# Performance work log

Hardware: AMD Instinct MI355X
Metric: run time of the kernel (lower is better)

Reference implementation:

```python
import jax, jax.numpy as jnp
import numpy as np


def setup_inputs() -> dict:
    key = jax.random.key(0)
    ks = jax.random.split(key, 9)
    B, S, E, H, D = 8, 1000, 1024, 16, 64
    sc = 0.02
    return {
        "x": jax.random.normal(ks[0], (B, S, E), dtype=jnp.float32),
        "wq": jax.random.normal(ks[1], (H, E, D), dtype=jnp.float32) * sc,
        "bq": jax.random.normal(ks[2], (H, D), dtype=jnp.float32) * sc,
        "wk": jax.random.normal(ks[3], (H, E, D), dtype=jnp.float32) * sc,
        "bk": jax.random.normal(ks[4], (H, D), dtype=jnp.float32) * sc,
        "wv": jax.random.normal(ks[5], (H, E, D), dtype=jnp.float32) * sc,
        "bv": jax.random.normal(ks[6], (H, D), dtype=jnp.float32) * sc,
        "wp": jax.random.normal(ks[7], (E, E), dtype=jnp.float32) * sc,
        "bp": jax.random.normal(ks[8], (E,), dtype=jnp.float32) * sc,
    }


def reference(x, wq, bq, wk, bk, wv, bv, wp, bp):
    B, S, E = x.shape
    H, _, D = wq.shape
    # per-head projections, all heads batched: [B,H,S,D]
    q = jnp.einsum('bse,hed->bhsd', x, wq) + bq[None, :, None, :]
    k = jnp.einsum('bse,hed->bhsd', x, wk) + bk[None, :, None, :]
    v = jnp.einsum('bse,hed->bhsd', x, wv) + bv[None, :, None, :]
    # NOTE: original scales by sqrt(seq_len), not sqrt(head_dim)
    scores = jnp.einsum('bhsd,bhtd->bhst', q, k) / jnp.asarray(S, x.dtype) ** 0.5
    causal = jnp.tril(jnp.ones((S, S), dtype=bool))  # mask[:S,:S] == 1 keeps
    scores = jnp.where(causal, scores, jnp.asarray(-jnp.inf, x.dtype))
    attn = jax.nn.softmax(scores, axis=-1)
    z = jnp.einsum('bhst,bhtd->bhsd', attn, v)
    # concat heads in head order -> [B,S,E]
    y = z.transpose(0, 2, 1, 3).reshape(B, S, E)
    # projection then exact GELU (dropout is identity at eval)
    return jax.nn.gelu(jnp.einsum('bse,ef->bsf', y, wp) + bp, approximate=False)
```

## Files before the change

kernel.cpp:

```cpp
#include <hip/hip_runtime.h>
#include <hip/hip_bf16.h>
#include <math.h>

constexpr int B_ = 8, S_ = 1000, E_ = 1024, H_ = 16, D_ = 64;
constexpr int M_ = B_ * S_;

using bf16x8 = __attribute__((ext_vector_type(8))) __bf16;
using u16x8  = __attribute__((ext_vector_type(8))) unsigned short;
using f32x4  = __attribute__((ext_vector_type(4))) float;

static __device__ __forceinline__ unsigned short f2bf(float f) {
    union { float f; unsigned u; } c; c.f = f;
    return (unsigned short)((c.u + 0x7FFF + ((c.u >> 16) & 1)) >> 16);
}
static __device__ __forceinline__ unsigned short f2bf_fast(float f) {
    union { float f; unsigned u; } c; c.f = f;
    return (unsigned short)((c.u + 0x8000) >> 16);
}
static __device__ __forceinline__ float bfr2f(unsigned short s) {
    union { unsigned u; float f; } c; c.u = ((unsigned)s) << 16;
    return c.f;
}

static __device__ __forceinline__ void gld16(const unsigned short* g, unsigned short* lds) {
    __builtin_amdgcn_global_load_lds(
        (__attribute__((address_space(1))) void*)(g),
        (__attribute__((address_space(3))) void*)(lds), 16, 0, 0);
}

__global__ __launch_bounds__(256) void cast_x_kernel(
    const float* __restrict__ x, unsigned short* __restrict__ xbf)
{
    const size_t i = ((size_t)blockIdx.x * 256 + threadIdx.x) * 4;
    float4 v = *(const float4*)(x + i);
    ushort4 o;
    o.x = f2bf(v.x); o.y = f2bf(v.y); o.z = f2bf(v.z); o.w = f2bf(v.w);
    *(ushort4*)(xbf + i) = o;
}

__global__ __launch_bounds__(256) void transpose_wqkv_kernel(
    const float* __restrict__ wq, const float* __restrict__ wk,
    const float* __restrict__ wv, unsigned short* __restrict__ WT)
{
    __shared__ unsigned short Ts[64 * 65];
    const int et = blockIdx.x, zh = blockIdx.y;
    const int z = zh >> 4, h = zh & 15;
    const float* src = (z == 0 ? wq : z == 1 ? wk : wv) + (size_t)h * E_ * D_;

    const int d = threadIdx.x & 63;
    const int e0 = threadIdx.x >> 6;
    #pragma unroll
    for (int p = 0; p < 16; ++p) {
        const int e = e0 + p * 4;
        Ts[d * 65 + e] = f2bf(src[(size_t)(et * 64 + e) * D_ + d]);
    }
    __syncthreads();
    const int e = threadIdx.x & 63;
    const int d0 = threadIdx.x >> 6;
    #pragma unroll
    for (int p = 0; p < 16; ++p) {
        const int dd = d0 + p * 4;
        WT[((size_t)zh * 64 + dd) * E_ + et * 64 + e] = Ts[dd * 65 + e];
    }
}

__global__ __launch_bounds__(256) void transpose_wp_kernel(
    const float* __restrict__ wp, unsigned short* __restrict__ wpT)
{
    __shared__ unsigned short Ts[64 * 65];
    const int et = blockIdx.x, ft = blockIdx.y;
    const int f = threadIdx.x & 63;
    const int e0 = threadIdx.x >> 6;
    #pragma unroll
    for (int p = 0; p < 16; ++p) {
        const int e = e0 + p * 4;
        Ts[f * 65 + e] = f2bf(wp[(size_t)(et * 64 + e) * E_ + ft * 64 + f]);
    }
    __syncthreads();
    const int e = threadIdx.x & 63;
    const int f0 = threadIdx.x >> 6;
    #pragma unroll
    for (int p = 0; p < 16; ++p) {
        const int ff = f0 + p * 4;
        wpT[((size_t)(ft * 64 + ff)) * E_ + et * 64 + e] = Ts[ff * 65 + e];
    }
}

__global__ __launch_bounds__(256) void transpose_v_kernel(
    const unsigned short* __restrict__ vb, unsigned short* __restrict__ vt)
{
    __shared__ unsigned short Ts[64 * 65];
    const int st = blockIdx.x, bh = blockIdx.y;
    const size_t ibase = (size_t)bh * S_ * D_;
    const size_t obase = (size_t)bh * D_ * S_;

    const int d = threadIdx.x & 63;
    const int s0 = threadIdx.x >> 6;
    #pragma unroll
    for (int p = 0; p < 16; ++p) {
        const int s = s0 + p * 4;
        const int srow = st * 64 + s;
        Ts[s * 65 + d] = (srow < S_) ? vb[ibase + (size_t)srow * D_ + d] : 0;
    }
    __syncthreads();
    const int s = threadIdx.x & 63;
    const int d0 = threadIdx.x >> 6;
    const int scol = st * 64 + s;
    if (scol < S_) {
        #pragma unroll
        for (int p = 0; p < 16; ++p) {
            const int dd = d0 + p * 4;
            vt[obase + (size_t)dd * S_ + scol] = Ts[s * 65 + dd];
        }
    }
}

__global__ __launch_bounds__(256) void qkv_mfma_kernel(
    const unsigned short* __restrict__ xbf, const unsigned short* __restrict__ WT,
    const float* __restrict__ bq, const float* __restrict__ bk,
    const float* __restrict__ bv,
    unsigned short* __restrict__ qb, unsigned short* __restrict__ kb,
    unsigned short* __restrict__ vb)
{
    __shared__ unsigned short As[128 * 64];
    __shared__ unsigned short Bs[128 * 64];

    const int tid  = threadIdx.x;
    const int wave = tid >> 6, lane = tid & 63;
    const int m16  = lane & 15, quad = lane >> 4;
    const int wm   = wave >> 1, wn = wave & 1;
    const int n0   = blockIdx.x * 128;
    const int m0   = blockIdx.y * 128;

    f32x4 acc[4][4];
    #pragma unroll
    for (int nf = 0; nf < 4; ++nf)
        #pragma unroll
        for (int mf = 0; mf < 4; ++mf)
            acc[nf][mf] = (f32x4){0.f, 0.f, 0.f, 0.f};

    const int lrow = lane >> 3;
    const int lcol = (lane & 7) << 3;

    int a_srow[4];
    #pragma unroll
    for (int j = 0; j < 4; ++j) {
        int r = m0 + (wave * 4 + j) * 8 + lrow;
        a_srow[j] = (r < M_) ? r : (M_ - 1);
    }

    for (int kk = 0; kk < E_; kk += 64) {
        __syncthreads();
        #pragma unroll
        for (int j = 0; j < 4; ++j) {
            const int i = wave * 4 + j;
            gld16(xbf + (size_t)a_srow[j] * E_ + kk + lcol, &As[i * 512]);
            gld16(WT + (size_t)(n0 + i * 8 + lrow) * E_ + kk + lcol, &Bs[i * 512]);
        }
        __syncthreads();

        #pragma unroll
        for (int kh = 0; kh < 2; ++kh) {
            const int ko = kh * 32 + quad * 8;
            bf16x8 af[4];
            #pragma unroll
            for (int mf = 0; mf < 4; ++mf)
                af[mf] = *(const bf16x8*)&As[(wm * 64 + mf * 16 + m16) * 64 + ko];
            #pragma unroll
            for (int nf = 0; nf < 4; ++nf) {
                const bf16x8 bfr = *(const bf16x8*)&Bs[(wn * 64 + nf * 16 + m16) * 64 + ko];
                #pragma unroll
                for (int mf = 0; mf < 4; ++mf)
                    acc[nf][mf] = __builtin_amdgcn_mfma_f32_16x16x32_bf16(
                        af[mf], bfr, acc[nf][mf], 0, 0, 0);
            }
        }
    }

    const int z = n0 >> 10;
    const int h = ((n0 >> 6) + wn) & 15;
    unsigned short* const ob = (z == 0) ? qb : (z == 1) ? kb : vb;
    const float* const bz    = (z == 0) ? bq : (z == 1) ? bk : bv;

    float biasv[4];
    #pragma unroll
    for (int nf = 0; nf < 4; ++nf)
        biasv[nf] = bz[h * D_ + nf * 16 + m16];

    #pragma unroll
    for (int mf = 0; mf < 4; ++mf)
        #pragma unroll
        for (int r = 0; r < 4; ++r) {
            const int row = m0 + wm * 64 + mf * 16 + quad * 4 + r;
            if (row < M_) {
                const int b = row / S_, s = row % S_;
                const size_t obase = (((size_t)b * H_ + h) * S_ + s) * D_ + m16;
                #pragma unroll
                for (int nf = 0; nf < 4; ++nf)
                    ob[obase + nf * 16] = f2bf(acc[nf][mf][r] + biasv[nf]);
            }
        }
}

__global__ __launch_bounds__(256) void attn_flash_kernel(
    const unsigned short* __restrict__ q, const unsigned short* __restrict__ k,
    const unsigned short* __restrict__ vt, unsigned short* __restrict__ ybf)
{
    constexpr int P_ = 72;
    __shared__ unsigned short Qs[64 * P_];
    __shared__ unsigned short Ks[64 * P_];
    __shared__ unsigned short Vt[64 * P_];
    __shared__ unsigned short Ps[4][16 * P_];

    const int tid  = threadIdx.x;
    const int wave = tid >> 6, lane = tid & 63;
    const int m16  = lane & 15, quad = lane >> 4;
    const int qt = (int)gridDim.x - 1 - (int)blockIdx.x;
    const int h = blockIdx.y, b = blockIdx.z;
    const size_t bh  = ((size_t)b * H_ + h) * S_;
    const size_t vtb = ((size_t)b * H_ + h) * (size_t)D_ * S_;
    const float sl2e = 0.031622776601683794f * 1.4426950408889634f;

    const int c8 = (tid & 7) * 8;
    const int r0 = tid >> 3;

    #pragma unroll
    for (int rr = 0; rr < 64; rr += 32) {
        const int r = r0 + rr;
        const int srow = qt * 64 + r;
        u16x8 val = {0, 0, 0, 0, 0, 0, 0, 0};
        if (srow < S_) val = *(const u16x8*)(q + (bh + srow) * D_ + c8);
        u16x8 o;
        #pragma unroll
        for (int j = 0; j < 8; ++j) o[j] = f2bf_fast(bfr2f(val[j]) * sl2e);
        *(u16x8*)&Qs[r * P_ + c8] = o;
    }
    __syncthreads();

    const bf16x8 qa0 = *(const bf16x8*)&Qs[(wave * 16 + m16) * P_ + quad * 8];
    const bf16x8 qa1 = *(const bf16x8*)&Qs[(wave * 16 + m16) * P_ + 32 + quad * 8];

    f32x4 O[4] = {{0,0,0,0},{0,0,0,0},{0,0,0,0},{0,0,0,0}};
    float l_i[4] = {0.f, 0.f, 0.f, 0.f};

    const int qrow_base = qt * 64 + wave * 16 + quad * 4;

    u16x8 kreg[2], vreg[2];
    #pragma unroll
    for (int i = 0; i < 2; ++i) {
        const int srow = r0 + i * 32;
        kreg[i] = *(const u16x8*)(k + (bh + srow) * D_ + c8);
        vreg[i] = *(const u16x8*)(vt + vtb + (size_t)(r0 + i * 32) * S_ + c8);
    }

    for (int tt = 0; tt <= qt; ++tt) {
        const int t0 = tt * 64;
        __syncthreads();
        #pragma unroll
        for (int i = 0; i < 2; ++i) {
            *(u16x8*)&Ks[(r0 + i * 32) * P_ + c8] = kreg[i];
            *(u16x8*)&Vt[(r0 + i * 32) * P_ + c8] = vreg[i];
        }
        __syncthreads();

        if (tt < qt) {
            const int nt0 = t0 + 64;
            #pragma unroll
            for (int i = 0; i < 2; ++i) {
                const int t = r0 + i * 32;
                const int srow = nt0 + t;
                u16x8 kv = {0,0,0,0,0,0,0,0}, vv = {0,0,0,0,0,0,0,0};
                if (srow < S_) kv = *(const u16x8*)(k + (bh + srow) * D_ + c8);
                if (nt0 + c8 < S_)
                    vv = *(const u16x8*)(vt + vtb + (size_t)t * S_ + nt0 + c8);
                kreg[i] = kv; vreg[i] = vv;
            }
        }

        f32x4 sc[4];
        #pragma unroll
        for (int ts = 0; ts < 4; ++ts) {
            const bf16x8 kb0 = *(const bf16x8*)&Ks[(ts * 16 + m16) * P_ + quad * 8];
            const bf16x8 kb1 = *(const bf16x8*)&Ks[(ts * 16 + m16) * P_ + 32 + quad * 8];
            f32x4 a = {0.f, 0.f, 0.f, 0.f};
            a = __builtin_amdgcn_mfma_f32_16x16x32_bf16(qa0, kb0, a, 0, 0, 0);
            a = __builtin_amdgcn_mfma_f32_16x16x32_bf16(qa1, kb1, a, 0, 0, 0);
            sc[ts] = a;
        }

        unsigned short* const pw = &Ps[wave][0];
        if (tt == qt) {
            #pragma unroll
            for (int ts = 0; ts < 4; ++ts) {
                const int t = t0 + ts * 16 + m16;
                #pragma unroll
                for (int r = 0; r < 4; ++r) {
                    float p = __builtin_amdgcn_exp2f(sc[ts][r]);
                    p = (t <= qrow_base + r) ? p : 0.f;
                    pw[(quad * 4 + r) * P_ + ts * 16 + m16] = f2bf_fast(p);
                    l_i[r] += p;
                }
            }
        } else {
            #pragma unroll
            for (int ts = 0; ts < 4; ++ts)
                #pragma unroll
                for (int r = 0; r < 4; ++r) {
                    const float p = __builtin_amdgcn_exp2f(sc[ts][r]);
                    pw[(quad * 4 + r) * P_ + ts * 16 + m16] = f2bf_fast(p);
                    l_i[r] += p;
                }
        }

        const bf16x8 pa0 = *(const bf16x8*)&pw[m16 * P_ + quad * 8];
        const bf16x8 pa1 = *(const bf16x8*)&pw[m16 * P_ + 32 + quad * 8];
        #pragma unroll
        for (int db = 0; db < 4; ++db) {
            const bf16x8 vb0 = *(const bf16x8*)&Vt[(db * 16 + m16) * P_ + quad * 8];
            const bf16x8 vb1 = *(const bf16x8*)&Vt[(db * 16 + m16) * P_ + 32 + quad * 8];
            O[db] = __builtin_amdgcn_mfma_f32_16x16x32_bf16(pa0, vb0, O[db], 0, 0, 0);
            O[db] = __builtin_amdgcn_mfma_f32_16x16x32_bf16(pa1, vb1, O[db], 0, 0, 0);
        }
    }

    #pragma unroll
    for (int off = 1; off < 16; off <<= 1)
        #pragma unroll
        for (int r = 0; r < 4; ++r)
            l_i[r] += __shfl_xor(l_i[r], off, 64);

    #pragma unroll
    for (int r = 0; r < 4; ++r) {
        const int qrow = qrow_base + r;
        if (qrow < S_) {
            const float invl = 1.0f / l_i[r];
            #pragma unroll
            for (int db = 0; db < 4; ++db)
                ybf[((size_t)b * S_ + qrow) * E_ + h * D_ + db * 16 + m16] =
                    f2bf(O[db][r] * invl);
        }
    }
}

__global__ __launch_bounds__(256) void proj_mfma_kernel(
    const unsigned short* __restrict__ ybf, const unsigned short* __restrict__ wpT,
    const float* __restrict__ bp, float* __restrict__ out)
{
    constexpr int P = 72;
    __shared__ unsigned short As[128 * P];
    __shared__ unsigned short Bs[128 * P];

    const int tid = threadIdx.x;
    const int wave = tid >> 6, lane = tid & 63;
    const int m16 = lane & 15, quad = lane >> 4;
    const int wm = wave >> 1, wn = wave & 1;
    const int m0 = blockIdx.x * 128;
    const int n0 = blockIdx.y * 128;

    f32x4 acc[4][4];
    #pragma unroll
    for (int nf = 0; nf < 4; ++nf)
        #pragma unroll
        for (int mf = 0; mf < 4; ++mf)
            acc[nf][mf] = (f32x4){0.f, 0.f, 0.f, 0.f};

    const int ar = tid & 31;
    const int ac8 = (tid >> 5) * 8;

    int asrow[4];
    #pragma unroll
    for (int p = 0; p < 4; ++p) {
        int r = m0 + ar + p * 32;
        asrow[p] = (r < M_) ? r : (M_ - 1);
    }

    u16x8 areg[4], breg[4];
    #pragma unroll
    for (int p = 0; p < 4; ++p) {
        areg[p] = *(const u16x8*)(ybf + (size_t)asrow[p] * E_ + ac8);
        breg[p] = *(const u16x8*)(wpT + (size_t)(n0 + ar + p * 32) * E_ + ac8);
    }

    for (int kk = 0; kk < E_; kk += 64) {
        __syncthreads();
        #pragma unroll
        for (int p = 0; p < 4; ++p) {
            *(u16x8*)&As[(ar + p * 32) * P + ac8] = areg[p];
            *(u16x8*)&Bs[(ar + p * 32) * P + ac8] = breg[p];
        }
        __syncthreads();

        if (kk + 64 < E_) {
            const int kn = kk + 64;
            #pragma unroll
            for (int p = 0; p < 4; ++p) {
                areg[p] = *(const u16x8*)(ybf + (size_t)asrow[p] * E_ + kn + ac8);
                breg[p] = *(const u16x8*)(wpT + (size_t)(n0 + ar + p * 32) * E_ + kn + ac8);
            }
        }

        #pragma unroll
        for (int kh = 0; kh < 2; ++kh) {
            const int ko = kh * 32 + quad * 8;
            bf16x8 af[4];
            #pragma unroll
            for (int mf = 0; mf < 4; ++mf)
                af[mf] = *(const bf16x8*)&As[(wm * 64 + mf * 16 + m16) * P + ko];
            #pragma unroll
            for (int nf = 0; nf < 4; ++nf) {
                const bf16x8 bfr = *(const bf16x8*)&Bs[(wn * 64 + nf * 16 + m16) * P + ko];
                #pragma unroll
                for (int mf = 0; mf < 4; ++mf)
                    acc[nf][mf] = __builtin_amdgcn_mfma_f32_16x16x32_bf16(
                        af[mf], bfr, acc[nf][mf], 0, 0, 0);
            }
        }
    }

    float biasv[4];
    #pragma unroll
    for (int nf = 0; nf < 4; ++nf)
        biasv[nf] = bp[n0 + wn * 64 + nf * 16 + m16];

    #pragma unroll
    for (int mf = 0; mf < 4; ++mf)
        #pragma unroll
        for (int r = 0; r < 4; ++r) {
            const int row = m0 + wm * 64 + mf * 16 + quad * 4 + r;
            if (row < M_) {
                #pragma unroll
                for (int nf = 0; nf < 4; ++nf) {
                    const int col = n0 + wn * 64 + nf * 16 + m16;
                    const float t = acc[nf][mf][r] + biasv[nf];
                    const float g = 0.5f * t * (1.0f + erff(t * 0.70710678118654752f));
                    out[(size_t)row * E_ + col] = g;
                }
            }
        }
}

extern "C" void kernel_launch(void* const* d_in, const int* in_sizes, int n_in,
                              void* d_out, int out_size, void* d_ws, size_t ws_size,
                              hipStream_t stream)
{
    const float* x  = (const float*)d_in[0];
    const float* wq = (const float*)d_in[1];
    const float* bq = (const float*)d_in[2];
    const float* wk = (const float*)d_in[3];
    const float* bk = (const float*)d_in[4];
    const float* wv = (const float*)d_in[5];
    const float* bv = (const float*)d_in[6];
    const float* wp = (const float*)d_in[7];
    const float* bp = (const float*)d_in[8];
    float* out = (float*)d_out;

    const size_t nME = (size_t)M_ * E_;
    unsigned short* xbf = (unsigned short*)d_ws;
    unsigned short* WT  = xbf + nME;
    unsigned short* wpT = WT + 3145728;
    unsigned short* qb  = wpT + 1048576;
    unsigned short* kb  = qb + nME;
    unsigned short* vb  = kb + nME;
    unsigned short* ybf = vb + nME;
    unsigned short* vtr = ybf + nME;

    cast_x_kernel<<<dim3((unsigned)(nME / 1024)), 256, 0, stream>>>(x, xbf);
    transpose_wqkv_kernel<<<dim3(16, 48), 256, 0, stream>>>(wq, wk, wv, WT);
    transpose_wp_kernel<<<dim3(16, 16), 256, 0, stream>>>(wp, wpT);

    qkv_mfma_kernel<<<dim3(3072 / 128, (M_ + 127) / 128), 256, 0, stream>>>(
        xbf, WT, bq, bk, bv, qb, kb, vb);
    transpose_v_kernel<<<dim3(16, B_ * H_), 256, 0, stream>>>(vb, vtr);
    attn_flash_kernel<<<dim3((S_ + 63) / 64, H_, B_), 256, 0, stream>>>(
        qb, kb, vtr, ybf);
    proj_mfma_kernel<<<dim3((M_ + 127) / 128, E_ / 128), 256, 0, stream>>>(
        ybf, wpT, bp, out);
}
```

Before: 302.5 us.

## Add MFMA wave priority in attention and use direct-to-LDS loads in projection

The attention inner loop now raises wave priority with s_setprio around the QK^T and PV MFMA blocks so matrix work gets scheduled ahead of other waves. Separately, the projection GEMM drops its register-staged, padded-LDS prefetch and instead loads tiles straight into unpadded LDS through the gld16 helper. This aims to cut VGPR staging traffic and instruction count, but it gives up the software prefetch overlap. The unpadded 64-element row stride may also cause LDS bank conflicts on fragment reads.

```diff
diff --git a/kernel.cpp b/kernel.cpp
--- a/kernel.cpp
+++ b/kernel.cpp
@@ -278,6 +278,7 @@
         }
 
         f32x4 sc[4];
+        __builtin_amdgcn_s_setprio(1);
         #pragma unroll
         for (int ts = 0; ts < 4; ++ts) {
             const bf16x8 kb0 = *(const bf16x8*)&Ks[(ts * 16 + m16) * P_ + quad * 8];
@@ -287,6 +288,7 @@
             a = __builtin_amdgcn_mfma_f32_16x16x32_bf16(qa1, kb1, a, 0, 0, 0);
             sc[ts] = a;
         }
+        __builtin_amdgcn_s_setprio(0);
 
         unsigned short* const pw = &Ps[wave][0];
         if (tt == qt) {
@@ -314,6 +316,7 @@
 
         const bf16x8 pa0 = *(const bf16x8*)&pw[m16 * P_ + quad * 8];
         const bf16x8 pa1 = *(const bf16x8*)&pw[m16 * P_ + 32 + quad * 8];
+        __builtin_amdgcn_s_setprio(1);
         #pragma unroll
         for (int db = 0; db < 4; ++db) {
             const bf16x8 vb0 = *(const bf16x8*)&Vt[(db * 16 + m16) * P_ + quad * 8];
@@ -321,6 +324,7 @@
             O[db] = __builtin_amdgcn_mfma_f32_16x16x32_bf16(pa0, vb0, O[db], 0, 0, 0);
             O[db] = __builtin_amdgcn_mfma_f32_16x16x32_bf16(pa1, vb1, O[db], 0, 0, 0);
         }
+        __builtin_amdgcn_s_setprio(0);
     }
 
     #pragma unroll
@@ -346,9 +350,8 @@
     const unsigned short* __restrict__ ybf, const unsigned short* __restrict__ wpT,
     const float* __restrict__ bp, float* __restrict__ out)
 {
-    constexpr int P = 72;
-    __shared__ unsigned short As[128 * P];
-    __shared__ unsigned short Bs[128 * P];
+    __shared__ unsigned short As[128 * 64];
+    __shared__ unsigned short Bs[128 * 64];
 
     const int tid = threadIdx.x;
     const int wave = tid >> 6, lane = tid & 63;
@@ -364,40 +367,25 @@
         for (int mf = 0; mf < 4; ++mf)
             acc[nf][mf] = (f32x4){0.f, 0.f, 0.f, 0.f};
 
-    const int ar = tid & 31;
-    const int ac8 = (tid >> 5) * 8;
-
-    int asrow[4];
-    #pragma unroll
-    for (int p = 0; p < 4; ++p) {
-        int r = m0 + ar + p * 32;
-        asrow[p] = (r < M_) ? r : (M_ - 1);
-    }
-
-    u16x8 areg[4], breg[4];
-    #pragma unroll
-    for (int p = 0; p < 4; ++p) {
-        areg[p] = *(const u16x8*)(ybf + (size_t)asrow[p] * E_ + ac8);
-        breg[p] = *(const u16x8*)(wpT + (size_t)(n0 + ar + p * 32) * E_ + ac8);
+    const int lrow = lane >> 3;
+    const int lcol = (lane & 7) << 3;
+
+    int a_srow[4];
+    #pragma unroll
+    for (int j = 0; j < 4; ++j) {
+        int r = m0 + (wave * 4 + j) * 8 + lrow;
+        a_srow[j] = (r < M_) ? r : (M_ - 1);
     }
 
     for (int kk = 0; kk < E_; kk += 64) {
         __syncthreads();
         #pragma unroll
-        for (int p = 0; p < 4; ++p) {
-            *(u16x8*)&As[(ar + p * 32) * P + ac8] = areg[p];
-            *(u16x8*)&Bs[(ar + p * 32) * P + ac8] = breg[p];
-        }
-        __syncthreads();
-
-        if (kk + 64 < E_) {
-            const int kn = kk + 64;
-            #pragma unroll
-            for (int p = 0; p < 4; ++p) {
-                areg[p] = *(const u16x8*)(ybf + (size_t)asrow[p] * E_ + kn + ac8);
-                breg[p] = *(const u16x8*)(wpT + (size_t)(n0 + ar + p * 32) * E_ + kn + ac8);
-            }
-        }
+        for (int j = 0; j < 4; ++j) {
+            const int i = wave * 4 + j;
+            gld16(ybf + (size_t)a_srow[j] * E_ + kk + lcol, &As[i * 512]);
+            gld16(wpT + (size_t)(n0 + i * 8 + lrow) * E_ + kk + lcol, &Bs[i * 512]);
+        }
+        __syncthreads();
 
         #pragma unroll
         for (int kh = 0; kh < 2; ++kh) {
@@ -405,10 +393,10 @@
             bf16x8 af[4];
             #pragma unroll
             for (int mf = 0; mf < 4; ++mf)
-                af[mf] = *(const bf16x8*)&As[(wm * 64 + mf * 16 + m16) * P + ko];
+                af[mf] = *(const bf16x8*)&As[(wm * 64 + mf * 16 + m16) * 64 + ko];
             #pragma unroll
             for (int nf = 0; nf < 4; ++nf) {
-                const bf16x8 bfr = *(const bf16x8*)&Bs[(wn * 64 + nf * 16 + m16) * P + ko];
+                const bf16x8 bfr = *(const bf16x8*)&Bs[(wn * 64 + nf * 16 + m16) * 64 + ko];
                 #pragma unroll
                 for (int mf = 0; mf < 4; ++mf)
                     acc[nf][mf] = __builtin_amdgcn_mfma_f32_16x16x32_bf16(
```

Result: no change. 298.3 us (-1.4%).
